# Kernel optimization log

Hardware: AMD Instinct MI355X
Metric: run time of the kernel (lower is better)

## Reference

```python
import jax, jax.numpy as jnp
import numpy as np

DIM = 384
HEADS = 12
WH, WW = 7, 7
N = WH * WW
HEAD_DIM = DIM // HEADS
SCALE = HEAD_DIM ** -0.5


def _double_step_seq(step1, len1, step2, len2):
    seq1 = np.arange(0, step1 * len1, step1)
    seq2 = np.arange(0, step2 * len2, step2)
    return (seq1[:, None] + seq2[None, :]).reshape(1, -1)


def _rel_position_index():
    coords = _double_step_seq(2 * WW - 1, WH, 1, WW)  # (1, N)
    idx = coords + coords.T                            # (N, N)
    idx = idx[:, ::-1].copy()                          # flip along dim 1
    return jnp.asarray(idx, dtype=jnp.int32)

REL_IDX = _rel_position_index()


def setup_inputs() -> dict:
    key = jax.random.key(0)
    ks = jax.random.split(key, 6)
    B_ = 4096
    x = jax.random.normal(ks[0], (B_, N, DIM), dtype=jnp.float32)
    mask = jnp.zeros((64, N, N), dtype=jnp.float32)
    qkv_w = jax.random.normal(ks[1], (3 * DIM, DIM), dtype=jnp.float32) * 0.02
    qkv_b = jax.random.normal(ks[2], (3 * DIM,), dtype=jnp.float32) * 0.02
    proj_w = jax.random.normal(ks[3], (DIM, DIM), dtype=jnp.float32) * 0.02
    proj_b = jax.random.normal(ks[4], (DIM,), dtype=jnp.float32) * 0.02
    bias_table = jax.random.normal(ks[5], (169, HEADS), dtype=jnp.float32) * 0.02
    return {"x": x, "mask": mask, "qkv_w": qkv_w, "qkv_b": qkv_b,
            "proj_w": proj_w, "proj_b": proj_b, "bias_table": bias_table}


def reference(x, mask, qkv_w, qkv_b, proj_w, proj_b, bias_table):
    B_, n, C = x.shape
    # qkv projection: (B_, N, 3C) -> (3, B_, H, N, d)
    qkv = (x @ qkv_w.T + qkv_b).reshape(B_, n, 3, HEADS, HEAD_DIM)
    qkv = jnp.transpose(qkv, (2, 0, 3, 1, 4))
    q, k, v = qkv[0], qkv[1], qkv[2]
    q = q * SCALE
    attn = jnp.einsum('bhnd,bhmd->bhnm', q, k)  # (B_, H, N, N)
    # gathered relative position bias: (H, N, N)
    rel_bias = bias_table[REL_IDX.reshape(-1)].reshape(n, n, HEADS)
    rel_bias = jnp.transpose(rel_bias, (2, 0, 1))
    attn = attn + rel_bias[None]
    nW = mask.shape[0]
    attn = attn.reshape(B_ // nW, nW, HEADS, n, n) + mask[None, :, None]
    attn = attn.reshape(B_, HEADS, n, n)
    attn = jax.nn.softmax(attn, axis=-1)
    out = jnp.einsum('bhnm,bhmd->bnhd', attn, v).reshape(B_, n, C)
    out = out @ proj_w.T + proj_b
    return out
```

## Files before the change

### kernel.cpp

```cpp
#include <hip/hip_runtime.h>
#include <hip/hip_bf16.h>

#define NTOK 49
#define DIMC 384
#define NH 12
#define QSCALE 0.17677669529663687f

typedef __attribute__((ext_vector_type(8))) short short8;
typedef __attribute__((ext_vector_type(4))) float f32x4;
typedef unsigned int u32;

#define WQB2_SHORTS (54 * 8192)
#define WPB_SHORTS  (18 * 8192)

__device__ __forceinline__ short f2bf(float f) {
    __bf16 h = (__bf16)f;
    return __builtin_bit_cast(short, h);
}
__device__ __forceinline__ float bf2f(short s) {
    u32 u = ((u32)(unsigned short)s) << 16;
    return __builtin_bit_cast(float, u);
}
__device__ __forceinline__ int cof(int p) { return 13 * (p / 7) + (p % 7); }

__device__ __forceinline__ void gld_lds16(const void* g, void* l) {
    __builtin_amdgcn_global_load_lds(
        (const __attribute__((address_space(1))) u32*)g,
        (__attribute__((address_space(3))) u32*)l, 16, 0, 0);
}

__device__ __forceinline__ short8 gather_bf(const float* __restrict__ w, int row, int k0) {
    const float* p = w + row * DIMC + k0;
    float4 a = *(const float4*)p;
    float4 b = *(const float4*)(p + 4);
    short8 r;
    r[0]=f2bf(a.x); r[1]=f2bf(a.y); r[2]=f2bf(a.z); r[3]=f2bf(a.w);
    r[4]=f2bf(b.x); r[5]=f2bf(b.y); r[6]=f2bf(b.z); r[7]=f2bf(b.w);
    return r;
}

__global__ void prep2(const float* __restrict__ qw, const float* __restrict__ pw,
                      short* __restrict__ wqb2, short* __restrict__ wpb) {
    int gt = blockIdx.x * 256 + threadIdx.x;
    int tile = gt >> 10;
    int rem = gt & 1023;
    int r = rem >> 3, g = rem & 7;
    int kc = tile % 6;
    int k0 = kc * 64 + ((g ^ (r & 7)) << 3);
    short8 o;
    if (tile < 54) {
        int nb = tile / 6;
        const float* src = qw + (size_t)(nb * 128 + r) * DIMC + k0;
        #pragma unroll
        for (int e = 0; e < 8; ++e) o[e] = f2bf(src[e]);
        *(short8*)(wqb2 + (size_t)tile * 8192 + r * 64 + g * 8) = o;
    } else {
        int t2 = tile - 54;
        int nb = t2 / 6;
        const float* src = pw + (size_t)(nb * 128 + r) * DIMC + k0;
        #pragma unroll
        for (int e = 0; e < 8; ++e) o[e] = f2bf(src[e]);
        *(short8*)(wpb + (size_t)t2 * 8192 + r * 64 + g * 8) = o;
    }
}

__global__ __launch_bounds__(1024)
void prep_x(const float* __restrict__ x, short* __restrict__ xa, int w0) {
    const int bid = blockIdx.x;
    const int mt = bid / 6, kc = bid % 6;
    const int tid = threadIdx.x;
    const int r = tid >> 3, g = tid & 7;
    const int win = w0 + mt * 2 + (r >> 6);
    const int tok = r & 63;
    const int k0 = kc * 64 + ((g ^ (r & 7)) << 3);
    short8 o;
    if (tok < NTOK) {
        const float* src = x + ((size_t)win * NTOK + tok) * DIMC + k0;
        float4 a = *(const float4*)src;
        float4 b = *(const float4*)(src + 4);
        o[0]=f2bf(a.x); o[1]=f2bf(a.y); o[2]=f2bf(a.z); o[3]=f2bf(a.w);
        o[4]=f2bf(b.x); o[5]=f2bf(b.y); o[6]=f2bf(b.z); o[7]=f2bf(b.w);
    } else {
        o = (short8)0;
    }
    *(short8*)(xa + ((size_t)mt * 6 + kc) * 8192 + r * 64 + g * 8) = o;
}

__global__ __launch_bounds__(256, 2)
void qkv_gemm(const short* __restrict__ xa, const float* __restrict__ qkv_b,
              const short* __restrict__ wqb2, short* __restrict__ qkvb)
{
    __shared__ char LC[2][32768] __attribute__((aligned(128)));

    const int tid = threadIdx.x;
    const int wv = tid >> 6, lane = tid & 63;
    const int l15 = lane & 15, l4 = lane >> 4;
    const int wr = wv >> 1, wc = wv & 1;
    const int sg = blockIdx.x / 72, bb = blockIdx.x % 72;
    const int mb = sg * 8 + (bb & 7), nb = bb >> 3;

    const char* asrc = (const char*)xa + (size_t)mb * 6 * 16384;
    const char* bsrc = (const char*)wqb2 + (size_t)(nb * 6) * 8192 * 2;

    f32x4 acc[4][4];
    #pragma unroll
    for (int mi = 0; mi < 4; ++mi)
        #pragma unroll
        for (int ni = 0; ni < 4; ++ni) acc[mi][ni] = (f32x4){0.f, 0.f, 0.f, 0.f};

    #pragma unroll
    for (int it = 0; it < 4; ++it) {
        int L = (wv * 4 + it) * 1024;
        gld_lds16(asrc + L + lane * 16, &LC[0][L]);
        gld_lds16(bsrc + L + lane * 16, &LC[0][16384 + L]);
    }

    #pragma unroll
    for (int kc = 0; kc < 6; ++kc) {
        __builtin_amdgcn_sched_barrier(0);
        asm volatile("s_waitcnt vmcnt(0)" ::: "memory");
        __builtin_amdgcn_s_barrier();
        __builtin_amdgcn_sched_barrier(0);
        if (kc < 5) {
            #pragma unroll
            for (int it = 0; it < 4; ++it) {
                int L = (wv * 4 + it) * 1024;
                gld_lds16(asrc + (kc + 1) * 16384 + L + lane * 16, &LC[(kc + 1) & 1][L]);
                gld_lds16(bsrc + (kc + 1) * 16384 + L + lane * 16, &LC[(kc + 1) & 1][16384 + L]);
            }
        }
        const char* bufp = LC[kc & 1];
        __builtin_amdgcn_s_setprio(1);
        #pragma unroll
        for (int ksub = 0; ksub < 2; ++ksub) {
            short8 a[4], b[4];
            #pragma unroll
            for (int mi = 0; mi < 4; ++mi) {
                int row = wr * 64 + mi * 16 + l15;
                a[mi] = *(const short8*)(bufp + row * 128 +
                        ((ksub * 64 + l4 * 16) ^ ((row & 7) << 4)));
            }
            #pragma unroll
            for (int ni = 0; ni < 4; ++ni) {
                int row = wc * 64 + ni * 16 + l15;
                b[ni] = *(const short8*)(bufp + 16384 + row * 128 +
                        ((ksub * 64 + l4 * 16) ^ ((row & 7) << 4)));
            }
            #pragma unroll
            for (int mi = 0; mi < 4; ++mi)
                #pragma unroll
                for (int ni = 0; ni < 4; ++ni)
                    acc[mi][ni] = __builtin_amdgcn_mfma_f32_16x16x32_bf16(
                        a[mi], b[ni], acc[mi][ni], 0, 0, 0);
        }
        __builtin_amdgcn_s_setprio(0);
    }

    __syncthreads();

    float bias[4];
    #pragma unroll
    for (int ni = 0; ni < 4; ++ni) bias[ni] = qkv_b[nb * 128 + wc * 64 + ni * 16 + l15];

    char* slab = (char*)LC + wv * 8192;
    const int wl = mb * 2 + wr;
    const int sub = nb / 3;

    if (sub < 2) {
        #pragma unroll
        for (int mi = 0; mi < 4; ++mi)
            #pragma unroll
            for (int ni = 0; ni < 4; ++ni)
                #pragma unroll
                for (int reg = 0; reg < 4; ++reg) {
                    float v = acc[mi][ni][reg] + bias[ni];
                    if (sub == 0) v *= QSCALE;
                    int rowp = mi * 16 + l4 * 4 + reg, colp = ni * 16 + l15;
                    *(short*)(slab + rowp * 128 + ((colp * 2) ^ ((rowp & 7) << 4))) = f2bf(v);
                }
        __builtin_amdgcn_sched_barrier(0);
        asm volatile("s_waitcnt lgkmcnt(0)" ::: "memory");
        __builtin_amdgcn_sched_barrier(0);
        #pragma unroll
        for (int hh = 0; hh < 2; ++hh)
            #pragma unroll
            for (int s = 0; s < 4; ++s) {
                int head = (nb % 3) * 4 + wc * 2 + hh;
                int rowp = s * 16 + l15;
                short8 frag = *(const short8*)(slab + rowp * 128 +
                              ((hh * 64 + l4 * 16) ^ ((rowp & 7) << 4)));
                *(short8*)(qkvb + (((size_t)wl * NH + head) * 12 + sub * 4 + s) * 512 + lane * 8) = frag;
            }
    } else {
        #pragma unroll
        for (int mi = 0; mi < 4; ++mi)
            #pragma unroll
            for (int ni = 0; ni < 4; ++ni)
                #pragma unroll
                for (int reg = 0; reg < 4; ++reg) {
                    float v = acc[mi][ni][reg] + bias[ni];
                    int rowp = mi * 16 + l4 * 4 + reg, colp = ni * 16 + l15;
                    *(short*)(slab + colp * 128 + ((rowp * 2) ^ ((colp & 7) << 4))) = f2bf(v);
                }
        __builtin_amdgcn_sched_barrier(0);
        asm volatile("s_waitcnt lgkmcnt(0)" ::: "memory");
        __builtin_amdgcn_sched_barrier(0);
        #pragma unroll
        for (int hh = 0; hh < 2; ++hh)
            #pragma unroll
            for (int dt = 0; dt < 2; ++dt)
                #pragma unroll
                for (int kst = 0; kst < 2; ++kst) {
                    int head = (nb - 6) * 4 + wc * 2 + hh;
                    int row2 = hh * 32 + dt * 16 + l15;
                    short8 frag = *(const short8*)(slab + row2 * 128 +
                                  ((kst * 64 + l4 * 16) ^ ((row2 & 7) << 4)));
                    *(short8*)(qkvb + (((size_t)wl * NH + head) * 12 + 8 + dt * 2 + kst) * 512 + lane * 8) = frag;
                }
    }
}

__global__ __launch_bounds__(256)
void attn_win(const float* __restrict__ mask, const float* __restrict__ bias_table,
              const short* __restrict__ qkvb, char* __restrict__ avb, int w0)
{
    __shared__ short SA[6144] __attribute__((aligned(128)));
    const int PS2 = 0, BT2 = 4096;

    const int tid = threadIdx.x;
    const int wv = tid >> 6, lane = tid & 63;
    const int l15 = lane & 15, l4 = lane >> 4;
    const int wl = blockIdx.x;
    const int win = w0 + wl;

    for (int i = tid; i < 169 * NH; i += 256) SA[BT2 + i] = f2bf(bias_table[i]);

    u32 mvp[4][2];
    int bidx[4][4];
    {
        const float* maskp = mask + (size_t)(win & 63) * (NTOK * NTOK);
        #pragma unroll
        for (int t = 0; t < 4; ++t) {
            int m = t * 16 + l15;
            float pad = (m < NTOK) ? 0.f : -1e30f;
            #pragma unroll
            for (int rp = 0; rp < 2; ++rp) {
                float v[2];
                #pragma unroll
                for (int e = 0; e < 2; ++e) {
                    int i = wv * 16 + l4 * 4 + rp * 2 + e;
                    v[e] = ((i < NTOK && m < NTOK) ? maskp[i * NTOK + m] : 0.f) + pad;
                }
                mvp[t][rp] = (u32)(unsigned short)f2bf(v[0]) |
                             ((u32)(unsigned short)f2bf(v[1]) << 16);
            }
        }
        int cofi[4], cofm[4];
        #pragma unroll
        for (int t = 0; t < 4; ++t) {
            int m = t * 16 + l15;
            cofm[t] = cof(48 - (m < NTOK ? m : 48));
        }
        #pragma unroll
        for (int reg = 0; reg < 4; ++reg) {
            int i = wv * 16 + l4 * 4 + reg;
            cofi[reg] = cof(i < NTOK ? i : 48);
        }
        #pragma unroll
        for (int t = 0; t < 4; ++t)
            #pragma unroll
            for (int reg = 0; reg < 4; ++reg)
                bidx[t][reg] = (cofi[reg] + cofm[t]) * NH;
    }
    const f32x4 zf = (f32x4){0.f, 0.f, 0.f, 0.f};
    __syncthreads();

    const short* qh = qkvb + (size_t)wl * (NH * 12 * 512);

    #pragma unroll 1
    for (int h = 0; h < NH; ++h) {
        const short* hb = qh + h * (12 * 512) + lane * 8;
        short8 q = *(const short8*)(hb + 0 * 512 + wv * 512);
        short8 kf[4], vf[4];
        #pragma unroll
        for (int t = 0; t < 4; ++t) kf[t] = *(const short8*)(hb + (4 + t) * 512);
        #pragma unroll
        for (int j = 0; j < 4; ++j) vf[j] = *(const short8*)(hb + (8 + j) * 512);

        f32x4 sc[4];
        #pragma unroll
        for (int t = 0; t < 4; ++t)
            sc[t] = __builtin_amdgcn_mfma_f32_16x16x32_bf16(q, kf[t], zf, 0, 0, 0);

        float p[4][4];
        #pragma unroll
        for (int t = 0; t < 4; ++t)
            #pragma unroll
            for (int reg = 0; reg < 4; ++reg) {
                u32 pk = mvp[t][reg >> 1];
                float mval = bf2f((short)((reg & 1) ? (pk >> 16) : (pk & 0xffff)));
                float bt = bf2f(SA[BT2 + bidx[t][reg] + h]);
                p[t][reg] = sc[t][reg] + mval + bt;
            }
        #pragma unroll
        for (int reg = 0; reg < 4; ++reg) {
            float mx = fmaxf(fmaxf(p[0][reg], p[1][reg]), fmaxf(p[2][reg], p[3][reg]));
            #pragma unroll
            for (int off = 8; off >= 1; off >>= 1) mx = fmaxf(mx, __shfl_xor(mx, off, 64));
            float s0 = 0.f;
            #pragma unroll
            for (int t = 0; t < 4; ++t) { p[t][reg] = __expf(p[t][reg] - mx); s0 += p[t][reg]; }
            #pragma unroll
            for (int off = 8; off >= 1; off >>= 1) s0 += __shfl_xor(s0, off, 64);
            float rs = 1.f / s0;
            #pragma unroll
            for (int t = 0; t < 4; ++t) p[t][reg] *= rs;
        }
        #pragma unroll
        for (int t = 0; t < 4; ++t)
            #pragma unroll
            for (int reg = 0; reg < 4; ++reg) {
                int r = l4 * 4 + reg;
                int byt = r * 128 + ((((t * 16 + l15) << 1)) ^ ((r & 7) << 4));
                SA[PS2 + wv * 1024 + (byt >> 1)] = f2bf(p[t][reg]);
            }
        f32x4 av[2];
        av[0] = zf; av[1] = zf;
        #pragma unroll
        for (int kst = 0; kst < 2; ++kst) {
            short8 pa;
            {
                int byt = l15 * 128 + (((kst * 64 + l4 * 16)) ^ ((l15 & 7) << 4));
                pa = *(const short8*)&SA[PS2 + wv * 1024 + (byt >> 1)];
            }
            #pragma unroll
            for (int dt = 0; dt < 2; ++dt)
                av[dt] = __builtin_amdgcn_mfma_f32_16x16x32_bf16(pa, vf[dt * 2 + kst], av[dt], 0, 0, 0);
        }
        #pragma unroll
        for (int dt = 0; dt < 2; ++dt)
            #pragma unroll
            for (int reg = 0; reg < 4; ++reg) {
                int tok = wv * 16 + l4 * 4 + reg;
                if (tok < NTOK) {
                    int r = (wl & 1) * 64 + tok;
                    int inner = ((((h & 1) << 6) | ((dt * 16 + l15) << 1))) ^ ((r & 7) << 4);
                    *(short*)(avb + (size_t)((wl >> 1) * 6 + (h >> 1)) * 16384 + r * 128 + inner)
                        = f2bf(av[dt][reg]);
                }
            }
    }
}

__global__ __launch_bounds__(256, 2)
void proj_pad(const char* __restrict__ avb, const short* __restrict__ wpb,
              const float* __restrict__ proj_b, float* __restrict__ out, int mb0)
{
    __shared__ char LC[2][32768] __attribute__((aligned(128)));

    const int tid = threadIdx.x;
    const int wv = tid >> 6, lane = tid & 63;
    const int l15 = lane & 15, l4 = lane >> 4;
    const int wr = wv >> 1, wc = wv & 1;
    const int sg = blockIdx.x / 24, bb = blockIdx.x % 24;
    const int mb = sg * 8 + (bb & 7), nb = bb >> 3;

    const char* asrc = avb + (size_t)mb * 6 * 16384;
    const char* bsrc = (const char*)wpb + (size_t)nb * 6 * 16384;

    f32x4 acc[4][4];
    #pragma unroll
    for (int mi = 0; mi < 4; ++mi)
        #pragma unroll
        for (int ni = 0; ni < 4; ++ni) acc[mi][ni] = (f32x4){0.f, 0.f, 0.f, 0.f};

    #pragma unroll
    for (int it = 0; it < 4; ++it) {
        int L = (wv * 4 + it) * 1024;
        gld_lds16(asrc + L + lane * 16, &LC[0][L]);
        gld_lds16(bsrc + L + lane * 16, &LC[0][16384 + L]);
    }

    #pragma unroll
    for (int kc = 0; kc < 6; ++kc) {
        __builtin_amdgcn_sched_barrier(0);
        asm volatile("s_waitcnt vmcnt(0)" ::: "memory");
        __builtin_amdgcn_s_barrier();
        __builtin_amdgcn_sched_barrier(0);
        if (kc < 5) {
            #pragma unroll
            for (int it = 0; it < 4; ++it) {
                int L = (wv * 4 + it) * 1024;
                gld_lds16(asrc + (kc + 1) * 16384 + L + lane * 16, &LC[(kc + 1) & 1][L]);
                gld_lds16(bsrc + (kc + 1) * 16384 + L + lane * 16, &LC[(kc + 1) & 1][16384 + L]);
            }
        }
        const char* bufp = LC[kc & 1];
        __builtin_amdgcn_s_setprio(1);
        #pragma unroll
        for (int ksub = 0; ksub < 2; ++ksub) {
            short8 a[4], b[4];
            #pragma unroll
            for (int mi = 0; mi < 4; ++mi) {
                int row = wr * 64 + mi * 16 + l15;
                a[mi] = *(const short8*)(bufp + row * 128 +
                        ((ksub * 64 + l4 * 16) ^ ((row & 7) << 4)));
            }
            #pragma unroll
            for (int ni = 0; ni < 4; ++ni) {
                int row = wc * 64 + ni * 16 + l15;
                b[ni] = *(const short8*)(bufp + 16384 + row * 128 +
                        ((ksub * 64 + l4 * 16) ^ ((row & 7) << 4)));
            }
            #pragma unroll
            for (int mi = 0; mi < 4; ++mi)
                #pragma unroll
                for (int ni = 0; ni < 4; ++ni)
                    acc[mi][ni] = __builtin_amdgcn_mfma_f32_16x16x32_bf16(
                        a[mi], b[ni], acc[mi][ni], 0, 0, 0);
        }
        __builtin_amdgcn_s_setprio(0);
    }

    float pb[4];
    #pragma unroll
    for (int ni = 0; ni < 4; ++ni) pb[ni] = proj_b[nb * 128 + wc * 64 + ni * 16 + l15];
    const int wg = (mb0 + mb) * 2 + wr;
    #pragma unroll
    for (int mi = 0; mi < 4; ++mi) {
        #pragma unroll
        for (int ni = 0; ni < 4; ++ni) {
            #pragma unroll
            for (int reg = 0; reg < 4; ++reg) {
                int tok = mi * 16 + l4 * 4 + reg;
                if (tok < NTOK)
                    out[((size_t)wg * NTOK + tok) * DIMC + nb * 128 + wc * 64 + ni * 16 + l15]
                        = acc[mi][ni][reg] + pb[ni];
            }
        }
    }
}

__global__ __launch_bounds__(256, 2)
void winattn_fallback(const float* __restrict__ x, const float* __restrict__ mask,
                      const float* __restrict__ qkv_w, const float* __restrict__ qkv_b,
                      const float* __restrict__ proj_w, const float* __restrict__ proj_b,
                      const float* __restrict__ bias_table, float* __restrict__ out)
{
    __shared__ short SL[26624] __attribute__((aligned(128)));
    const int tid = threadIdx.x, wv = tid >> 6, lane = tid & 63;
    const int l15 = lane & 15, l4 = lane >> 4;
    const int win = blockIdx.x;
    const int xbase = win * (NTOK * DIMC);
    const int KSo = 0, VTo = 2048, PSo = 4096, QAo = 8192;

    short8 xf[12];
    {
        const int row = wv * 16 + l15;
        const bool valid = row < NTOK;
        const float* xr = x + xbase + row * DIMC;
        #pragma unroll
        for (int ks = 0; ks < 12; ++ks)
            xf[ks] = valid ? gather_bf(xr, 0, ks * 32 + l4 * 8) : (short8)0;
    }
    float mv[4][4]; int bidx[4][4]; float negm[4];
    {
        const float* maskp = mask + (win & 63) * (NTOK * NTOK);
        int cofi[4], cofm[4];
        #pragma unroll
        for (int t = 0; t < 4; ++t) {
            int m = t * 16 + l15;
            negm[t] = (m < NTOK) ? 0.f : -1e30f;
            cofm[t] = cof(48 - (m < NTOK ? m : 48));
            #pragma unroll
            for (int reg = 0; reg < 4; ++reg) {
                int i = wv * 16 + l4 * 4 + reg;
                mv[t][reg] = (i < NTOK && m < NTOK) ? maskp[i * NTOK + m] : 0.f;
            }
        }
        #pragma unroll
        for (int reg = 0; reg < 4; ++reg) {
            int i = wv * 16 + l4 * 4 + reg;
            cofi[reg] = cof(i < NTOK ? i : 48);
        }
        #pragma unroll
        for (int t = 0; t < 4; ++t)
            #pragma unroll
            for (int reg = 0; reg < 4; ++reg) bidx[t][reg] = (cofi[reg] + cofm[t]) * NH;
    }
    f32x4 pacc[24];
    #pragma unroll
    for (int t = 0; t < 24; ++t) pacc[t] = (f32x4){0.f, 0.f, 0.f, 0.f};
    const f32x4 zf = (f32x4){0.f, 0.f, 0.f, 0.f};
    __syncthreads();

    #pragma unroll 1
    for (int h = 0; h < NH; ++h) {
        f32x4 qa[6];
        #pragma unroll
        for (int nt = 0; nt < 6; ++nt) qa[nt] = zf;
        #pragma unroll
        for (int nt = 0; nt < 6; ++nt) {
            const int grow = (nt >> 1) * DIMC + h * 32 + (nt & 1) * 16 + l15;
            #pragma unroll
            for (int ks = 0; ks < 12; ++ks) {
                short8 b = gather_bf(qkv_w, grow, ks * 32 + l4 * 8);
                qa[nt] = __builtin_amdgcn_mfma_f32_16x16x32_bf16(xf[ks], b, qa[nt], 0, 0, 0);
            }
        }
        #pragma unroll
        for (int nt = 0; nt < 6; ++nt) {
            const int sub = nt >> 1;
            const int colw = (nt & 1) * 16 + l15;
            const float bias = qkv_b[sub * DIMC + h * 32 + colw];
            #pragma unroll
            for (int reg = 0; reg < 4; ++reg) {
                const int tokg = wv * 16 + l4 * 4 + reg;
                float val = qa[nt][reg] + bias;
                if (sub == 0) {
                    int byt = tokg * 64 + ((colw << 1) ^ ((tokg & 3) << 4));
                    SL[QAo + (byt >> 1)] = f2bf(val * QSCALE);
                } else if (sub == 1) {
                    int byt = tokg * 64 + ((colw << 1) ^ ((tokg & 3) << 4));
                    SL[KSo + (byt >> 1)] = f2bf(val);
                } else {
                    int byt = colw * 128 + ((tokg << 1) ^ ((colw & 7) << 4));
                    SL[VTo + (byt >> 1)] = f2bf(val);
                }
            }
        }
        __syncthreads();
        short8 aq;
        { int row = wv*16+l15; int byt = row*64 + ((l4*16) ^ ((row&3)<<4));
          aq = *(const short8*)&SL[QAo + (byt>>1)]; }
        f32x4 sc[4];
        #pragma unroll
        for (int t = 0; t < 4; ++t) {
            int row = t*16+l15; int byt = row*64 + ((l4*16) ^ ((row&3)<<4));
            short8 bk = *(const short8*)&SL[KSo + (byt>>1)];
            sc[t] = __builtin_amdgcn_mfma_f32_16x16x32_bf16(aq, bk, zf, 0, 0, 0);
        }
        float p[4][4];
        #pragma unroll
        for (int t = 0; t < 4; ++t)
            #pragma unroll
            for (int reg = 0; reg < 4; ++reg)
                p[t][reg] = sc[t][reg] + mv[t][reg] + bias_table[bidx[t][reg] + h] + negm[t];
        #pragma unroll
        for (int reg = 0; reg < 4; ++reg) {
            float mx = fmaxf(fmaxf(p[0][reg], p[1][reg]), fmaxf(p[2][reg], p[3][reg]));
            #pragma unroll
            for (int off = 8; off >= 1; off >>= 1) mx = fmaxf(mx, __shfl_xor(mx, off, 64));
            float s0 = 0.f;
            #pragma unroll
            for (int t = 0; t < 4; ++t) { p[t][reg] = __expf(p[t][reg] - mx); s0 += p[t][reg]; }
            #pragma unroll
            for (int off = 8; off >= 1; off >>= 1) s0 += __shfl_xor(s0, off, 64);
            float rs = 1.f / s0;
            #pragma unroll
            for (int t = 0; t < 4; ++t) p[t][reg] *= rs;
        }
        #pragma unroll
        for (int t = 0; t < 4; ++t)
            #pragma unroll
            for (int reg = 0; reg < 4; ++reg) {
                int row = wv*16 + l4*4 + reg;
                int byt = row*128 + (((t*16+l15) << 1) ^ ((row&7)<<4));
                SL[PSo + (byt>>1)] = f2bf(p[t][reg]);
            }
        f32x4 av[2]; av[0] = zf; av[1] = zf;
        #pragma unroll
        for (int kst = 0; kst < 2; ++kst) {
            short8 pa;
            { int row = wv*16+l15; int byt = row*128 + ((kst*64+l4*16) ^ ((row&7)<<4));
              pa = *(const short8*)&SL[PSo + (byt>>1)]; }
            #pragma unroll
            for (int dt = 0; dt < 2; ++dt) {
                int d = dt*16+l15; int byt = d*128 + ((kst*64+l4*16) ^ ((d&7)<<4));
                short8 bv = *(const short8*)&SL[VTo + (byt>>1)];
                av[dt] = __builtin_amdgcn_mfma_f32_16x16x32_bf16(pa, bv, av[dt], 0, 0, 0);
            }
        }
        __syncthreads();
        #pragma unroll
        for (int dt = 0; dt < 2; ++dt)
            #pragma unroll
            for (int reg = 0; reg < 4; ++reg) {
                int row = wv*16 + l4*4 + reg;
                int byt = row*64 + (((dt*16+l15) << 1) ^ ((row&3)<<4));
                SL[QAo + (byt>>1)] = f2bf(av[dt][reg]);
            }
        __syncthreads();
        short8 aa;
        { int row = wv*16+l15; int byt = row*64 + ((l4*16) ^ ((row&3)<<4));
          aa = *(const short8*)&SL[QAo + (byt>>1)]; }
        #pragma unroll
        for (int nt = 0; nt < 24; ++nt) {
            short8 bp = gather_bf(proj_w, nt * 16 + l15, h * 32 + l4 * 8);
            pacc[nt] = __builtin_amdgcn_mfma_f32_16x16x32_bf16(aa, bp, pacc[nt], 0, 0, 0);
        }
    }
    {
        float* op = out + xbase;
        #pragma unroll
        for (int nt = 0; nt < 24; ++nt) {
            const float pb = proj_b[nt * 16 + l15];
            #pragma unroll
            for (int reg = 0; reg < 4; ++reg) {
                const int i = wv * 16 + l4 * 4 + reg;
                if (i < NTOK) op[i * DIMC + nt * 16 + l15] = pacc[nt][reg] + pb;
            }
        }
    }
}

extern "C" void kernel_launch(void* const* d_in, const int* in_sizes, int n_in,
                              void* d_out, int out_size, void* d_ws, size_t ws_size,
                              hipStream_t stream) {
    const float* x          = (const float*)d_in[0];
    const float* mask       = (const float*)d_in[1];
    const float* qkv_w      = (const float*)d_in[2];
    const float* qkv_b      = (const float*)d_in[3];
    const float* proj_w     = (const float*)d_in[4];
    const float* proj_b     = (const float*)d_in[5];
    const float* bias_table = (const float*)d_in[6];
    float* out = (float*)d_out;

    const size_t fixed = ((size_t)WQB2_SHORTS + WPB_SHORTS) * 2;
    auto need = [&](int c) {
        size_t wpc = 4096 / c;
        size_t mbc = wpc / 2;
        return fixed + mbc * 98304UL  + wpc * 147456UL  + mbc * 98304UL ;
    };
    int c = 0;
    if (ws_size >= need(8)) c = 8;
    else if (ws_size >= need(16)) c = 16;

    if (c) {
        short* wqb2 = (short*)d_ws;
        short* wpb  = wqb2 + WQB2_SHORTS;
        const int wpc = 4096 / c;
        const int mbc = wpc / 2;
        short* xa   = wpb + WPB_SHORTS;
        short* qkvb = xa + (size_t)mbc * 49152;
        char*  avb  = (char*)(qkvb + (size_t)wpc * 73728);

        prep2<<<288, 256, 0, stream>>>(qkv_w, proj_w, wqb2, wpb);
        for (int ch = 0; ch < c; ++ch) {
            const int w0 = ch * wpc;
            prep_x<<<mbc * 6, 1024, 0, stream>>>(x, xa, w0);
            qkv_gemm<<<mbc * 9, 256, 0, stream>>>(xa, qkv_b, wqb2, qkvb);
            attn_win<<<wpc, 256, 0, stream>>>(mask, bias_table, qkvb, avb, w0);
            proj_pad<<<mbc * 3, 256, 0, stream>>>(avb, wpb, proj_b, out, ch * mbc);
        }
    } else {
        winattn_fallback<<<4096, 256, 0, stream>>>(x, mask, qkv_w, qkv_b, proj_w,
                                                   proj_b, bias_table, out);
    }
}
```

Baseline: 809.2 us.

## Fuse window attention with output projection, keeping AV results in LDS

Merges the attention kernel and the projection GEMM into one 512-thread kernel. Each block handles two windows and keeps the attention output (bf16) in a 96KB LDS tile, then streams projection weight tiles through double-buffered LDS to compute the output directly. This drops the global round trip of the intermediate AV buffer and one kernel launch per chunk, and frees workspace so fewer, larger chunks (4) can be used. In exchange the large LDS footprint (~148KB) limits occupancy to one block per CU. Every block also re-reads the whole projection weight matrix for only 128 rows, which lowers weight reuse compared with the separate GEMM.

```diff
diff --git a/kernel.cpp b/kernel.cpp
--- a/kernel.cpp
+++ b/kernel.cpp
@@ -220,20 +220,29 @@
     }
 }
 
-__global__ __launch_bounds__(256)
-void attn_win(const float* __restrict__ mask, const float* __restrict__ bias_table,
-              const short* __restrict__ qkvb, char* __restrict__ avb, int w0)
+#define AVS_OFF 0
+#define PSW_OFF 98304
+#define BTT_OFF 114688
+#define BBB_OFF 118784
+#define APL_TOT 151552
+
+__global__ __launch_bounds__(512)
+void attnproj(const float* __restrict__ mask, const float* __restrict__ bias_table,
+              const short* __restrict__ qkvb, const short* __restrict__ wpb,
+              const float* __restrict__ proj_b, float* __restrict__ out, int w0)
 {
-    __shared__ short SA[6144] __attribute__((aligned(128)));
-    const int PS2 = 0, BT2 = 4096;
+    __shared__ char SB[APL_TOT] __attribute__((aligned(128)));
+    short* BT = (short*)(SB + BTT_OFF);
 
     const int tid = threadIdx.x;
     const int wv = tid >> 6, lane = tid & 63;
     const int l15 = lane & 15, l4 = lane >> 4;
-    const int wl = blockIdx.x;
-    const int win = w0 + wl;
-
-    for (int i = tid; i < 169 * NH; i += 256) SA[BT2 + i] = f2bf(bias_table[i]);
+    const int wl = wv >> 2;
+    const int st4 = wv & 3;
+    const int lw = blockIdx.x * 2 + wl;
+    const int win = w0 + lw;
+
+    for (int i = tid; i < 169 * NH; i += 512) BT[i] = f2bf(bias_table[i]);
 
     u32 mvp[4][2];
     int bidx[4][4];
@@ -248,7 +257,7 @@
                 float v[2];
                 #pragma unroll
                 for (int e = 0; e < 2; ++e) {
-                    int i = wv * 16 + l4 * 4 + rp * 2 + e;
+                    int i = st4 * 16 + l4 * 4 + rp * 2 + e;
                     v[e] = ((i < NTOK && m < NTOK) ? maskp[i * NTOK + m] : 0.f) + pad;
                 }
                 mvp[t][rp] = (u32)(unsigned short)f2bf(v[0]) |
@@ -263,7 +272,7 @@
         }
         #pragma unroll
         for (int reg = 0; reg < 4; ++reg) {
-            int i = wv * 16 + l4 * 4 + reg;
+            int i = st4 * 16 + l4 * 4 + reg;
             cofi[reg] = cof(i < NTOK ? i : 48);
         }
         #pragma unroll
@@ -275,12 +284,13 @@
     const f32x4 zf = (f32x4){0.f, 0.f, 0.f, 0.f};
     __syncthreads();
 
-    const short* qh = qkvb + (size_t)wl * (NH * 12 * 512);
+    const short* qh = qkvb + (size_t)lw * (NH * 12 * 512);
+    char* psw = SB + PSW_OFF + wv * 2048;
 
     #pragma unroll 1
     for (int h = 0; h < NH; ++h) {
         const short* hb = qh + h * (12 * 512) + lane * 8;
-        short8 q = *(const short8*)(hb + 0 * 512 + wv * 512);
+        short8 q = *(const short8*)(hb + st4 * 512);
         short8 kf[4], vf[4];
         #pragma unroll
         for (int t = 0; t < 4; ++t) kf[t] = *(const short8*)(hb + (4 + t) * 512);
@@ -299,7 +309,7 @@
             for (int reg = 0; reg < 4; ++reg) {
                 u32 pk = mvp[t][reg >> 1];
                 float mval = bf2f((short)((reg & 1) ? (pk >> 16) : (pk & 0xffff)));
-                float bt = bf2f(SA[BT2 + bidx[t][reg] + h]);
+                float bt = bf2f(BT[bidx[t][reg] + h]);
                 p[t][reg] = sc[t][reg] + mval + bt;
             }
         #pragma unroll
@@ -322,7 +332,7 @@
             for (int reg = 0; reg < 4; ++reg) {
                 int r = l4 * 4 + reg;
                 int byt = r * 128 + ((((t * 16 + l15) << 1)) ^ ((r & 7) << 4));
-                SA[PS2 + wv * 1024 + (byt >> 1)] = f2bf(p[t][reg]);
+                *(short*)(psw + byt) = f2bf(p[t][reg]);
             }
         f32x4 av[2];
         av[0] = zf; av[1] = zf;
@@ -331,7 +341,7 @@
             short8 pa;
             {
                 int byt = l15 * 128 + (((kst * 64 + l4 * 16)) ^ ((l15 & 7) << 4));
-                pa = *(const short8*)&SA[PS2 + wv * 1024 + (byt >> 1)];
+                pa = *(const short8*)(psw + byt);
             }
             #pragma unroll
             for (int dt = 0; dt < 2; ++dt)
@@ -341,102 +351,89 @@
         for (int dt = 0; dt < 2; ++dt)
             #pragma unroll
             for (int reg = 0; reg < 4; ++reg) {
-                int tok = wv * 16 + l4 * 4 + reg;
+                int tok = st4 * 16 + l4 * 4 + reg;
                 if (tok < NTOK) {
-                    int r = (wl & 1) * 64 + tok;
-                    int inner = ((((h & 1) << 6) | ((dt * 16 + l15) << 1))) ^ ((r & 7) << 4);
-                    *(short*)(avb + (size_t)((wl >> 1) * 6 + (h >> 1)) * 16384 + r * 128 + inner)
-                        = f2bf(av[dt][reg]);
+                    int row = wl * 64 + tok;
+                    int lb = (h * 32 + dt * 16 + l15) * 2;
+                    *(short*)(SB + AVS_OFF + row * 768 + (lb ^ ((row & 7) << 4))) = f2bf(av[dt][reg]);
                 }
             }
     }
-}
-
-__global__ __launch_bounds__(256, 2)
-void proj_pad(const char* __restrict__ avb, const short* __restrict__ wpb,
-              const float* __restrict__ proj_b, float* __restrict__ out, int mb0)
-{
-    __shared__ char LC[2][32768] __attribute__((aligned(128)));
-
-    const int tid = threadIdx.x;
-    const int wv = tid >> 6, lane = tid & 63;
-    const int l15 = lane & 15, l4 = lane >> 4;
-    const int wr = wv >> 1, wc = wv & 1;
-    const int sg = blockIdx.x / 24, bb = blockIdx.x % 24;
-    const int mb = sg * 8 + (bb & 7), nb = bb >> 3;
-
-    const char* asrc = avb + (size_t)mb * 6 * 16384;
-    const char* bsrc = (const char*)wpb + (size_t)nb * 6 * 16384;
-
-    f32x4 acc[4][4];
+
+    asm volatile("s_waitcnt lgkmcnt(0)" ::: "memory");
+    __builtin_amdgcn_s_barrier();
+    __builtin_amdgcn_sched_barrier(0);
+
+    const char* bsrc = (const char*)wpb;
+    char* BB = SB + BBB_OFF;
+
     #pragma unroll
-    for (int mi = 0; mi < 4; ++mi)
-        #pragma unroll
-        for (int ni = 0; ni < 4; ++ni) acc[mi][ni] = (f32x4){0.f, 0.f, 0.f, 0.f};
-
+    for (int it = 0; it < 2; ++it) {
+        int L = it * 8192 + wv * 1024;
+        gld_lds16(bsrc + L + lane * 16, BB + L);
+    }
+
+    f32x4 acc[4][2];
     #pragma unroll
-    for (int it = 0; it < 4; ++it) {
-        int L = (wv * 4 + it) * 1024;
-        gld_lds16(asrc + L + lane * 16, &LC[0][L]);
-        gld_lds16(bsrc + L + lane * 16, &LC[0][16384 + L]);
-    }
-
-    #pragma unroll
-    for (int kc = 0; kc < 6; ++kc) {
+    for (int mi = 0; mi < 4; ++mi) { acc[mi][0] = zf; acc[mi][1] = zf; }
+
+    #pragma unroll 1
+    for (int t = 0; t < 18; ++t) {
+        const int kc = t % 6, nb = t / 6;
         __builtin_amdgcn_sched_barrier(0);
         asm volatile("s_waitcnt vmcnt(0)" ::: "memory");
         __builtin_amdgcn_s_barrier();
         __builtin_amdgcn_sched_barrier(0);
-        if (kc < 5) {
-            #pragma unroll
-            for (int it = 0; it < 4; ++it) {
-                int L = (wv * 4 + it) * 1024;
-                gld_lds16(asrc + (kc + 1) * 16384 + L + lane * 16, &LC[(kc + 1) & 1][L]);
-                gld_lds16(bsrc + (kc + 1) * 16384 + L + lane * 16, &LC[(kc + 1) & 1][16384 + L]);
-            }
-        }
-        const char* bufp = LC[kc & 1];
+        if (t < 17) {
+            #pragma unroll
+            for (int it = 0; it < 2; ++it) {
+                int L = it * 8192 + wv * 1024;
+                gld_lds16(bsrc + (size_t)(t + 1) * 16384 + L + lane * 16,
+                          BB + ((t + 1) & 1) * 16384 + L);
+            }
+        }
+        const char* bufp = BB + (t & 1) * 16384;
         __builtin_amdgcn_s_setprio(1);
         #pragma unroll
         for (int ksub = 0; ksub < 2; ++ksub) {
-            short8 a[4], b[4];
+            short8 a[4], b[2];
             #pragma unroll
             for (int mi = 0; mi < 4; ++mi) {
-                int row = wr * 64 + mi * 16 + l15;
-                a[mi] = *(const short8*)(bufp + row * 128 +
-                        ((ksub * 64 + l4 * 16) ^ ((row & 7) << 4)));
-            }
-            #pragma unroll
-            for (int ni = 0; ni < 4; ++ni) {
-                int row = wc * 64 + ni * 16 + l15;
-                b[ni] = *(const short8*)(bufp + 16384 + row * 128 +
+                int row = wl * 64 + mi * 16 + l15;
+                a[mi] = *(const short8*)(SB + AVS_OFF + row * 768 +
+                        ((kc * 128 + ksub * 64 + l4 * 16) ^ ((row & 7) << 4)));
+            }
+            #pragma unroll
+            for (int ni = 0; ni < 2; ++ni) {
+                int row = st4 * 32 + ni * 16 + l15;
+                b[ni] = *(const short8*)(bufp + row * 128 +
                         ((ksub * 64 + l4 * 16) ^ ((row & 7) << 4)));
             }
             #pragma unroll
             for (int mi = 0; mi < 4; ++mi)
                 #pragma unroll
-                for (int ni = 0; ni < 4; ++ni)
+                for (int ni = 0; ni < 2; ++ni)
                     acc[mi][ni] = __builtin_amdgcn_mfma_f32_16x16x32_bf16(
                         a[mi], b[ni], acc[mi][ni], 0, 0, 0);
         }
         __builtin_amdgcn_s_setprio(0);
-    }
-
-    float pb[4];
-    #pragma unroll
-    for (int ni = 0; ni < 4; ++ni) pb[ni] = proj_b[nb * 128 + wc * 64 + ni * 16 + l15];
-    const int wg = (mb0 + mb) * 2 + wr;
-    #pragma unroll
-    for (int mi = 0; mi < 4; ++mi) {
-        #pragma unroll
-        for (int ni = 0; ni < 4; ++ni) {
-            #pragma unroll
-            for (int reg = 0; reg < 4; ++reg) {
-                int tok = mi * 16 + l4 * 4 + reg;
-                if (tok < NTOK)
-                    out[((size_t)wg * NTOK + tok) * DIMC + nb * 128 + wc * 64 + ni * 16 + l15]
-                        = acc[mi][ni][reg] + pb[ni];
-            }
+        if (kc == 5) {
+            const int gw = win;
+            #pragma unroll
+            for (int ni = 0; ni < 2; ++ni) {
+                const int col = nb * 128 + st4 * 32 + ni * 16 + l15;
+                const float pb = proj_b[col];
+                #pragma unroll
+                for (int mi = 0; mi < 4; ++mi)
+                    #pragma unroll
+                    for (int reg = 0; reg < 4; ++reg) {
+                        int tok = mi * 16 + l4 * 4 + reg;
+                        if (tok < NTOK)
+                            out[((size_t)gw * NTOK + tok) * DIMC + col] = acc[mi][ni][reg] + pb;
+                    }
+            }
+            #pragma unroll
+            for (int mi = 0; mi < 4; ++mi) { acc[mi][0] = zf; acc[mi][1] = zf; }
         }
     }
 }
@@ -463,10 +460,11 @@
         for (int ks = 0; ks < 12; ++ks)
             xf[ks] = valid ? gather_bf(xr, 0, ks * 32 + l4 * 8) : (short8)0;
     }
-    float mv[4][4]; int bidx[4][4]; float negm[4];
+    float mv[4][4]; int bidx[4][4];
     {
         const float* maskp = mask + (win & 63) * (NTOK * NTOK);
         int cofi[4], cofm[4];
+        float negm[4];
         #pragma unroll
         for (int t = 0; t < 4; ++t) {
             int m = t * 16 + l15;
@@ -475,7 +473,7 @@
             #pragma unroll
             for (int reg = 0; reg < 4; ++reg) {
                 int i = wv * 16 + l4 * 4 + reg;
-                mv[t][reg] = (i < NTOK && m < NTOK) ? maskp[i * NTOK + m] : 0.f;
+                mv[t][reg] = ((i < NTOK && m < NTOK) ? maskp[i * NTOK + m] : 0.f) + negm[t];
             }
         }
         #pragma unroll
@@ -545,7 +543,7 @@
         for (int t = 0; t < 4; ++t)
             #pragma unroll
             for (int reg = 0; reg < 4; ++reg)
-                p[t][reg] = sc[t][reg] + mv[t][reg] + bias_table[bidx[t][reg] + h] + negm[t];
+                p[t][reg] = sc[t][reg] + mv[t][reg] + bias_table[bidx[t][reg] + h];
         #pragma unroll
         for (int reg = 0; reg < 4; ++reg) {
             float mx = fmaxf(fmaxf(p[0][reg], p[1][reg]), fmaxf(p[2][reg], p[3][reg]));
@@ -630,10 +628,11 @@
     auto need = [&](int c) {
         size_t wpc = 4096 / c;
         size_t mbc = wpc / 2;
-        return fixed + mbc * 98304UL  + wpc * 147456UL  + mbc * 98304UL ;
+        return fixed + mbc * 98304UL  + wpc * 147456UL ;
     };
     int c = 0;
-    if (ws_size >= need(8)) c = 8;
+    if (ws_size >= need(4)) c = 4;
+    else if (ws_size >= need(8)) c = 8;
     else if (ws_size >= need(16)) c = 16;
 
     if (c) {
@@ -643,15 +642,13 @@
         const int mbc = wpc / 2;
         short* xa   = wpb + WPB_SHORTS;
         short* qkvb = xa + (size_t)mbc * 49152;
-        char*  avb  = (char*)(qkvb + (size_t)wpc * 73728);
 
         prep2<<<288, 256, 0, stream>>>(qkv_w, proj_w, wqb2, wpb);
         for (int ch = 0; ch < c; ++ch) {
             const int w0 = ch * wpc;
             prep_x<<<mbc * 6, 1024, 0, stream>>>(x, xa, w0);
             qkv_gemm<<<mbc * 9, 256, 0, stream>>>(xa, qkv_b, wqb2, qkvb);
-            attn_win<<<wpc, 256, 0, stream>>>(mask, bias_table, qkvb, avb, w0);
-            proj_pad<<<mbc * 3, 256, 0, stream>>>(avb, wpb, proj_b, out, ch * mbc);
+            attnproj<<<mbc, 512, 0, stream>>>(mask, bias_table, qkvb, wpb, proj_b, out, w0);
         }
     } else {
         winattn_fallback<<<4096, 256, 0, stream>>>(x, mask, qkv_w, qkv_b, proj_w,
```

Result: faster. 784.8 us (-3.0%).
